# Optimization experiments

Measured on AMD Instinct MI355X. Metric: run time of the kernel, lower is better.

## Reference

```python
import jax, jax.numpy as jnp
import numpy as np

TEMPERATURE = 0.1
EPS = 1e-8  # torch F.cosine_similarity denom clamp


def setup_inputs() -> dict:
    key = jax.random.key(0)
    k1, k2, k3 = jax.random.split(key, 3)
    B, M, D, K = 8, 256, 768, 100
    N = B * M
    transformer_outputs = jax.random.normal(k1, (B, M, D), dtype=jnp.float32)
    cnn_targets = jax.random.normal(k2, (B, M, D), dtype=jnp.float32)
    # uniform sampling with replacement over [0, N) excluding self (multinomial on uniform mask)
    r = jax.random.randint(k3, (N, K), 0, N - 1)
    i = jnp.arange(N)[:, None]
    neg_indices = (r + (r >= i)).astype(jnp.int32)
    return {"transformer_outputs": transformer_outputs, "cnn_targets": cnn_targets, "neg_indices": neg_indices}


def reference(transformer_outputs, cnn_targets, neg_indices):
    B, M, D = transformer_outputs.shape
    N = B * M
    preds = transformer_outputs.reshape(N, D)
    targets = cnn_targets.reshape(N, D)
    pn = preds / jnp.clip(jnp.linalg.norm(preds, axis=-1, keepdims=True), EPS)
    tn = targets / jnp.clip(jnp.linalg.norm(targets, axis=-1, keepdims=True), EPS)
    # all pairwise cosine sims [N, N]; positive on the diagonal, negatives gathered by index
    sim = pn @ tn.T
    pos = jnp.diagonal(sim)                                   # [N]
    neg = sim[jnp.arange(N)[:, None], neg_indices]            # [N, K]
    logits = jnp.concatenate([pos[:, None], neg], axis=1) / TEMPERATURE
    # cross-entropy with label 0 for every row
    loss = -jnp.mean(jax.nn.log_softmax(logits, axis=-1)[:, 0])
    return loss
```

## Files before the change

kernel.cpp:

```cpp
#include <hip/hip_runtime.h>
#include <hip/hip_bf16.h>
#include <math.h>

#define NROWS 2048
#define DDIM  768
#define KNEG  100
#define NLOGITS 101
#define MT 7
#define KW 6

typedef __attribute__((ext_vector_type(4))) float floatx4;

static constexpr float TEMP_INV = 10.0f;
static constexpr float EPS_NORM = 1e-8f;

__device__ __forceinline__ unsigned pack_fp8x4(float a, float b, float c, float d) {
    int u = 0;
    u = __builtin_amdgcn_cvt_pk_fp8_f32(a, b, u, false);
    u = __builtin_amdgcn_cvt_pk_fp8_f32(c, d, u, true);
    return (unsigned)u;
}

__global__ __launch_bounds__(256) void cl_prep_kernel(
        const float* __restrict__ targets,
        unsigned char* __restrict__ tn8) {
    const int wave = threadIdx.x >> 6, lane = threadIdx.x & 63;
    const int row = blockIdx.x * 4 + wave;
    const float4* tv = (const float4*)(targets + (size_t)row * DDIM);
    const float4 a0 = tv[2 * lane], a1 = tv[2 * lane + 1], b0 = tv[128 + lane];

    float ss = 0.f;
    ss = fmaf(a0.x, a0.x, ss); ss = fmaf(a0.y, a0.y, ss);
    ss = fmaf(a0.z, a0.z, ss); ss = fmaf(a0.w, a0.w, ss);
    ss = fmaf(a1.x, a1.x, ss); ss = fmaf(a1.y, a1.y, ss);
    ss = fmaf(a1.z, a1.z, ss); ss = fmaf(a1.w, a1.w, ss);
    ss = fmaf(b0.x, b0.x, ss); ss = fmaf(b0.y, b0.y, ss);
    ss = fmaf(b0.z, b0.z, ss); ss = fmaf(b0.w, b0.w, ss);
    #pragma unroll
    for (int off = 32; off > 0; off >>= 1) ss += __shfl_xor(ss, off);
    const float it = 1.0f / fmaxf(sqrtf(ss), EPS_NORM);

    const unsigned u0 = pack_fp8x4(a0.x * it, a0.y * it, a0.z * it, a0.w * it);
    const unsigned u1 = pack_fp8x4(a1.x * it, a1.y * it, a1.z * it, a1.w * it);
    const unsigned u2 = pack_fp8x4(b0.x * it, b0.y * it, b0.z * it, b0.w * it);

    __shared__ __align__(16) unsigned char buf[4][DDIM];
    *(uint2*)(&buf[wave][8 * lane]) = make_uint2(u0, u1);
    *(unsigned*)(&buf[wave][512 + 4 * lane]) = u2;
    __syncthreads();
    if (lane < 48)
        ((uint4*)(tn8 + (size_t)row * DDIM))[lane] = *(const uint4*)(&buf[wave][16 * lane]);
}

__global__ __launch_bounds__(256, 4) void cl_rowloss_kernel(
        const float* __restrict__ preds,
        const unsigned char* __restrict__ tn8,
        const int* __restrict__ neg_idx,
        float* __restrict__ row_loss) {
    const int i = blockIdx.x;
    const int tid = threadIdx.x;
    const int wave = tid >> 6, lane = tid & 63;

    __shared__ __align__(16) unsigned char Ab[3][16 * DDIM];
    __shared__ __align__(16) unsigned char pn8[DDIM];
    __shared__ __align__(16) float parts[4][MT * 16];
    __shared__ int idx_lds[MT * 16];
    __shared__ float sP[4];

    if (tid < MT * 16)
        idx_lds[tid] = (tid == 0 || tid > KNEG) ? i : neg_idx[(size_t)i * KNEG + tid - 1];
    __syncthreads();

    auto stage = [&](int t, int buf, int nchunk) {
        #pragma unroll
        for (int it = 0; it < 3; ++it) {
            const int g = it * 256 + wave * 64 + lane;
            if (g < nchunk) {
                const int r = g / 48, c = g - r * 48;
                const unsigned char* src = tn8 + (size_t)idx_lds[t * 16 + r] * DDIM
                                           + ((c ^ (r & 7)) << 4);
                __builtin_amdgcn_global_load_lds(
                    (const __attribute__((address_space(1))) void*)src,
                    (__attribute__((address_space(3))) void*)&Ab[buf][(it * 256 + wave * 64) << 4],
                    16, 0, 0);
            }
        }
    };

    float4 pv4;
    if (tid < 192)
        pv4 = ((const float4*)(preds + (size_t)i * DDIM))[tid];

    stage(0, 0, 768);
    stage(1, 1, 768);

    if (tid < 192) {
        float ss = 0.f;
        ss = fmaf(pv4.x, pv4.x, ss); ss = fmaf(pv4.y, pv4.y, ss);
        ss = fmaf(pv4.z, pv4.z, ss); ss = fmaf(pv4.w, pv4.w, ss);
        #pragma unroll
        for (int off = 32; off > 0; off >>= 1) ss += __shfl_xor(ss, off);
        if (lane == 0) sP[wave] = ss;
    }
    asm volatile("s_waitcnt lgkmcnt(0)" ::: "memory");
    __builtin_amdgcn_s_barrier();
    __builtin_amdgcn_sched_barrier(0);

    if (tid < 192) {
        const float inv = 1.0f / fmaxf(sqrtf(sP[0] + sP[1] + sP[2]), EPS_NORM);
        ((unsigned*)pn8)[tid] = pack_fp8x4(pv4.x * inv, pv4.y * inv,
                                           pv4.z * inv, pv4.w * inv);
    }
    asm volatile("s_waitcnt lgkmcnt(0)" ::: "memory");
    __builtin_amdgcn_s_barrier();
    __builtin_amdgcn_sched_barrier(0);

    const int kb = wave * KW;
    const int q = lane >> 4;
    long long bfr[KW];
    #pragma unroll
    for (int kk = 0; kk < KW; ++kk)
        bfr[kk] = *(const long long*)(&pn8[(kb + kk) * 32 + q * 8]);

    const int aoff = (lane & 15) * DDIM + kb * 32 + q * 8;
    const int axor = (lane & 7) << 4;

    floatx4 acc[MT] = {};

#define CL_ITER(T, NWAIT, NC)                                                 \
    {                                                                         \
        if ((T) + 2 < MT) stage((T) + 2, ((T) + 2) % 3, NC);                  \
        asm volatile("s_waitcnt vmcnt(" #NWAIT ")" ::: "memory");             \
        __builtin_amdgcn_s_barrier();                                         \
        __builtin_amdgcn_sched_barrier(0);                                    \
        _Pragma("unroll")                                                     \
        for (int kk = 0; kk < KW; ++kk) {                                     \
            const long long af =                                              \
                *(const long long*)(&Ab[(T) % 3][(aoff + kk * 32) ^ axor]);   \
            acc[T] = __builtin_amdgcn_mfma_f32_16x16x32_fp8_fp8(af, bfr[kk],  \
                                                                acc[T], 0, 0, 0); \
        }                                                                     \
        asm volatile("s_waitcnt lgkmcnt(0)" ::: "memory");                    \
        __builtin_amdgcn_s_barrier();                                         \
        __builtin_amdgcn_sched_barrier(0);                                    \
    }

    CL_ITER(0, 6, 768)
    CL_ITER(1, 6, 768)
    CL_ITER(2, 6, 768)
    CL_ITER(3, 6, 768)
    CL_ITER(4, 4, 240)
    CL_ITER(5, 1, 0)
    CL_ITER(6, 0, 0)
#undef CL_ITER

    if ((lane & 15) == 0) {
        const int rb = q * 4;
        #pragma unroll
        for (int t = 0; t < MT; ++t)
            *(floatx4*)(&parts[wave][t * 16 + rb]) = acc[t];
    }
    __syncthreads();

    if (wave == 0) {
        const float v0 = (parts[0][lane] + parts[1][lane] +
                          parts[2][lane] + parts[3][lane]) * TEMP_INV;
        float v1 = -INFINITY;
        if (lane <= NLOGITS - 65)
            v1 = (parts[0][64 + lane] + parts[1][64 + lane] +
                  parts[2][64 + lane] + parts[3][64 + lane]) * TEMP_INV;
        const float l0 = __shfl(v0, 0);
        float m = fmaxf(v0, v1);
        #pragma unroll
        for (int off = 32; off > 0; off >>= 1) m = fmaxf(m, __shfl_xor(m, off));
        float e = expf(v0 - m);
        if (lane <= NLOGITS - 65) e += expf(v1 - m);
        #pragma unroll
        for (int off = 32; off > 0; off >>= 1) e += __shfl_xor(e, off);
        if (lane == 0) row_loss[i] = (m + logf(e)) - l0;
    }
}

__global__ void cl_reduce_kernel(const float* __restrict__ row_loss,
                                 float* __restrict__ out) {
    const int tid = threadIdx.x;
    float s = 0.f;
    #pragma unroll
    for (int c = 0; c < 2; ++c) {
        const float4 v = ((const float4*)row_loss)[tid + 256 * c];
        s += (v.x + v.y) + (v.z + v.w);
    }
    #pragma unroll
    for (int off = 32; off > 0; off >>= 1) s += __shfl_down(s, off);
    __shared__ float sw[4];
    const int wave = tid >> 6, lane = tid & 63;
    if (lane == 0) sw[wave] = s;
    __syncthreads();
    if (tid == 0) out[0] = (sw[0] + sw[1] + sw[2] + sw[3]) / (float)NROWS;
}

extern "C" void kernel_launch(void* const* d_in, const int* in_sizes, int n_in,
                              void* d_out, int out_size, void* d_ws, size_t ws_size,
                              hipStream_t stream) {
    const float* preds   = (const float*)d_in[0];
    const float* targets = (const float*)d_in[1];
    const int*   neg_idx = (const int*)d_in[2];
    float* out = (float*)d_out;

    unsigned char* tn8 = (unsigned char*)d_ws;
    float* row_loss = (float*)((char*)d_ws + (size_t)NROWS * DDIM);

    cl_prep_kernel<<<NROWS / 4, 256, 0, stream>>>(targets, tn8);
    cl_rowloss_kernel<<<NROWS, 256, 0, stream>>>(preds, tn8, neg_idx, row_loss);
    cl_reduce_kernel<<<1, 256, 0, stream>>>(row_loss, out);
}
```

Baseline: 25.67 us.

## Quantize normalized targets to FP4 and use scaled 16x16x128 MFMA

```diff
diff --git a/kernel.cpp b/kernel.cpp
--- a/kernel.cpp
+++ b/kernel.cpp
@@ -4,14 +4,16 @@
 
 #define NROWS 2048
 #define DDIM  768
+#define TNB   384
 #define KNEG  100
 #define NLOGITS 101
 #define MT 7
-#define KW 6
 
 typedef __attribute__((ext_vector_type(4))) float floatx4;
-
-static constexpr float TEMP_INV = 10.0f;
+typedef __attribute__((ext_vector_type(4))) int   intx4;
+typedef __attribute__((ext_vector_type(8))) int   intx8;
+
+static constexpr float LFAC = 10.0f / 32.0f;
 static constexpr float EPS_NORM = 1e-8f;
 
 __device__ __forceinline__ unsigned pack_fp8x4(float a, float b, float c, float d) {
@@ -21,9 +23,16 @@
     return (unsigned)u;
 }
 
+__device__ __forceinline__ unsigned fp4n(float v) {
+    const float a = fminf(fabsf(v), 6.0f);
+    const unsigned c = (a >= 0.25f) + (a >= 0.75f) + (a >= 1.25f) + (a >= 1.75f)
+                     + (a >= 2.5f)  + (a >= 3.5f)  + (a >= 5.0f);
+    return c | (v < 0.f ? 8u : 0u);
+}
+
 __global__ __launch_bounds__(256) void cl_prep_kernel(
         const float* __restrict__ targets,
-        unsigned char* __restrict__ tn8) {
+        unsigned char* __restrict__ tn4) {
     const int wave = threadIdx.x >> 6, lane = threadIdx.x & 63;
     const int row = blockIdx.x * 4 + wave;
     const float4* tv = (const float4*)(targets + (size_t)row * DDIM);
@@ -38,47 +47,54 @@
     ss = fmaf(b0.z, b0.z, ss); ss = fmaf(b0.w, b0.w, ss);
     #pragma unroll
     for (int off = 32; off > 0; off >>= 1) ss += __shfl_xor(ss, off);
-    const float it = 1.0f / fmaxf(sqrtf(ss), EPS_NORM);
-
-    const unsigned u0 = pack_fp8x4(a0.x * it, a0.y * it, a0.z * it, a0.w * it);
-    const unsigned u1 = pack_fp8x4(a1.x * it, a1.y * it, a1.z * it, a1.w * it);
-    const unsigned u2 = pack_fp8x4(b0.x * it, b0.y * it, b0.z * it, b0.w * it);
-
-    __shared__ __align__(16) unsigned char buf[4][DDIM];
-    *(uint2*)(&buf[wave][8 * lane]) = make_uint2(u0, u1);
-    *(unsigned*)(&buf[wave][512 + 4 * lane]) = u2;
-    __syncthreads();
-    if (lane < 48)
-        ((uint4*)(tn8 + (size_t)row * DDIM))[lane] = *(const uint4*)(&buf[wave][16 * lane]);
-}
-
-__global__ __launch_bounds__(256, 4) void cl_rowloss_kernel(
+    const float sc = 32.0f / fmaxf(sqrtf(ss), EPS_NORM);
+
+    const unsigned ua =  fp4n(a0.x * sc)        | (fp4n(a0.y * sc) << 4)
+                      | (fp4n(a0.z * sc) << 8)  | (fp4n(a0.w * sc) << 12)
+                      | (fp4n(a1.x * sc) << 16) | (fp4n(a1.y * sc) << 20)
+                      | (fp4n(a1.z * sc) << 24) | (fp4n(a1.w * sc) << 28);
+    const unsigned short ub = (unsigned short)(fp4n(b0.x * sc)
+                      | (fp4n(b0.y * sc) << 4) | (fp4n(b0.z * sc) << 8)
+                      | (fp4n(b0.w * sc) << 12));
+
+    __shared__ __align__(16) unsigned char buf[4][TNB];
+    *(unsigned*)(&buf[wave][4 * lane]) = ua;
+    *(unsigned short*)(&buf[wave][256 + 2 * lane]) = ub;
+    __syncthreads();
+    if (lane < 24)
+        ((uint4*)(tn4 + (size_t)row * TNB))[lane] = *(const uint4*)(&buf[wave][16 * lane]);
+}
+
+__global__ __launch_bounds__(256, 5) void cl_rowloss_kernel(
         const float* __restrict__ preds,
-        const unsigned char* __restrict__ tn8,
+        const unsigned char* __restrict__ tn4,
         const int* __restrict__ neg_idx,
         float* __restrict__ row_loss) {
     const int i = blockIdx.x;
     const int tid = threadIdx.x;
     const int wave = tid >> 6, lane = tid & 63;
-
-    __shared__ __align__(16) unsigned char Ab[3][16 * DDIM];
+    const int khalf = wave & 1, thalf = wave >> 1;
+    const int q = lane >> 4, rr = lane & 15;
+
+    __shared__ __align__(16) unsigned char Ab[2][32 * TNB];
     __shared__ __align__(16) unsigned char pn8[DDIM];
-    __shared__ __align__(16) float parts[4][MT * 16];
+    __shared__ __align__(16) float parts[2][MT * 16];
     __shared__ int idx_lds[MT * 16];
-    __shared__ float sP[4];
+    __shared__ float sP[3];
 
     if (tid < MT * 16)
         idx_lds[tid] = (tid == 0 || tid > KNEG) ? i : neg_idx[(size_t)i * KNEG + tid - 1];
     __syncthreads();
 
-    auto stage = [&](int t, int buf, int nchunk) {
+    auto stage = [&](int s, int buf, int nchunk) {
         #pragma unroll
         for (int it = 0; it < 3; ++it) {
             const int g = it * 256 + wave * 64 + lane;
             if (g < nchunk) {
-                const int r = g / 48, c = g - r * 48;
-                const unsigned char* src = tn8 + (size_t)idx_lds[t * 16 + r] * DDIM
-                                           + ((c ^ (r & 7)) << 4);
+                const int rl = g / 24, c = g - rl * 24;
+                const int slot = s * 16 + (rl < 16 ? rl : rl + 48);
+                const unsigned char* src = tn4 + (size_t)idx_lds[slot] * TNB
+                                           + ((c ^ (rl & 7)) << 4);
                 __builtin_amdgcn_global_load_lds(
                     (const __attribute__((address_space(1))) void*)src,
                     (__attribute__((address_space(3))) void*)&Ab[buf][(it * 256 + wave * 64) << 4],
@@ -88,16 +104,12 @@
     };
 
     float4 pv4;
-    if (tid < 192)
-        pv4 = ((const float4*)(preds + (size_t)i * DDIM))[tid];
-
+    if (tid < 192) pv4 = ((const float4*)(preds + (size_t)i * DDIM))[tid];
     stage(0, 0, 768);
-    stage(1, 1, 768);
 
     if (tid < 192) {
-        float ss = 0.f;
-        ss = fmaf(pv4.x, pv4.x, ss); ss = fmaf(pv4.y, pv4.y, ss);
-        ss = fmaf(pv4.z, pv4.z, ss); ss = fmaf(pv4.w, pv4.w, ss);
+        float ss = fmaf(pv4.x, pv4.x, fmaf(pv4.y, pv4.y,
+                   fmaf(pv4.z, pv4.z, pv4.w * pv4.w)));
         #pragma unroll
         for (int off = 32; off > 0; off >>= 1) ss += __shfl_xor(ss, off);
         if (lane == 0) sP[wave] = ss;
@@ -105,70 +117,68 @@
     asm volatile("s_waitcnt lgkmcnt(0)" ::: "memory");
     __builtin_amdgcn_s_barrier();
     __builtin_amdgcn_sched_barrier(0);
-
     if (tid < 192) {
         const float inv = 1.0f / fmaxf(sqrtf(sP[0] + sP[1] + sP[2]), EPS_NORM);
         ((unsigned*)pn8)[tid] = pack_fp8x4(pv4.x * inv, pv4.y * inv,
                                            pv4.z * inv, pv4.w * inv);
     }
-    asm volatile("s_waitcnt lgkmcnt(0)" ::: "memory");
-    __builtin_amdgcn_s_barrier();
-    __builtin_amdgcn_sched_barrier(0);
-
-    const int kb = wave * KW;
-    const int q = lane >> 4;
-    long long bfr[KW];
-    #pragma unroll
-    for (int kk = 0; kk < KW; ++kk)
-        bfr[kk] = *(const long long*)(&pn8[(kb + kk) * 32 + q * 8]);
-
-    const int aoff = (lane & 15) * DDIM + kb * 32 + q * 8;
-    const int axor = (lane & 7) << 4;
-
-    floatx4 acc[MT] = {};
-
-#define CL_ITER(T, NWAIT, NC)                                                 \
+    __syncthreads();
+
+    intx8 b8[3];
+    #pragma unroll
+    for (int m = 0; m < 3; ++m) {
+        const int boff = khalf * 384 + m * 128 + q * 32;
+        const intx4 lo = *(const intx4*)(&pn8[boff]);
+        const intx4 hi = *(const intx4*)(&pn8[boff + 16]);
+        b8[m] = (intx8){lo.x, lo.y, lo.z, lo.w, hi.x, hi.y, hi.z, hi.w};
+    }
+
+    floatx4 acc[4] = {};
+    const int rbase = (thalf * 16 + rr) * TNB;
+    const int rx = rr & 7;
+
+#define CL_S(S, NC_NEXT, DO_STAGE)                                            \
     {                                                                         \
-        if ((T) + 2 < MT) stage((T) + 2, ((T) + 2) % 3, NC);                  \
-        asm volatile("s_waitcnt vmcnt(" #NWAIT ")" ::: "memory");             \
-        __builtin_amdgcn_s_barrier();                                         \
-        __builtin_amdgcn_sched_barrier(0);                                    \
-        _Pragma("unroll")                                                     \
-        for (int kk = 0; kk < KW; ++kk) {                                     \
-            const long long af =                                              \
-                *(const long long*)(&Ab[(T) % 3][(aoff + kk * 32) ^ axor]);   \
-            acc[T] = __builtin_amdgcn_mfma_f32_16x16x32_fp8_fp8(af, bfr[kk],  \
-                                                                acc[T], 0, 0, 0); \
+        if (DO_STAGE) stage((S) + 1, ((S) + 1) & 1, NC_NEXT);                 \
+        if (!thalf || (S) < 3) {                                              \
+            _Pragma("unroll")                                                 \
+            for (int m = 0; m < 3; ++m) {                                     \
+                const int cl = khalf * 12 + m * 4 + q;                        \
+                const intx4 a4 = *(const intx4*)(&Ab[(S) & 1][rbase + ((cl ^ rx) << 4)]); \
+                const intx8 a8 = (intx8){a4.x, a4.y, a4.z, a4.w, 0, 0, 0, 0}; \
+                acc[S] = __builtin_amdgcn_mfma_scale_f32_16x16x128_f8f6f4(    \
+                    a8, b8[m], acc[S], 4 , 0 ,              \
+                    0, 127, 0, 127);                                          \
+            }                                                                 \
         }                                                                     \
-        asm volatile("s_waitcnt lgkmcnt(0)" ::: "memory");                    \
-        __builtin_amdgcn_s_barrier();                                         \
-        __builtin_amdgcn_sched_barrier(0);                                    \
-    }
-
-    CL_ITER(0, 6, 768)
-    CL_ITER(1, 6, 768)
-    CL_ITER(2, 6, 768)
-    CL_ITER(3, 6, 768)
-    CL_ITER(4, 4, 240)
-    CL_ITER(5, 1, 0)
-    CL_ITER(6, 0, 0)
-#undef CL_ITER
-
-    if ((lane & 15) == 0) {
+        __syncthreads();                                                      \
+    }
+
+    CL_S(0, 768, 1)
+    CL_S(1, 768, 1)
+    CL_S(2, 384, 1)
+    CL_S(3, 0, 0)
+#undef CL_S
+
+    if (rr == 0) {
         const int rb = q * 4;
-        #pragma unroll
-        for (int t = 0; t < MT; ++t)
-            *(floatx4*)(&parts[wave][t * 16 + rb]) = acc[t];
+        if (!thalf) {
+            #pragma unroll
+            for (int t = 0; t < 4; ++t)
+                *(floatx4*)(&parts[khalf][t * 16 + rb]) = acc[t];
+        } else {
+            #pragma unroll
+            for (int t = 0; t < 3; ++t)
+                *(floatx4*)(&parts[khalf][(t + 4) * 16 + rb]) = acc[t];
+        }
     }
     __syncthreads();
 
     if (wave == 0) {
-        const float v0 = (parts[0][lane] + parts[1][lane] +
-                          parts[2][lane] + parts[3][lane]) * TEMP_INV;
+        const float v0 = (parts[0][lane] + parts[1][lane]) * LFAC;
         float v1 = -INFINITY;
         if (lane <= NLOGITS - 65)
-            v1 = (parts[0][64 + lane] + parts[1][64 + lane] +
-                  parts[2][64 + lane] + parts[3][64 + lane]) * TEMP_INV;
+            v1 = (parts[0][64 + lane] + parts[1][64 + lane]) * LFAC;
         const float l0 = __shfl(v0, 0);
         float m = fmaxf(v0, v1);
         #pragma unroll
@@ -207,10 +217,10 @@
     const int*   neg_idx = (const int*)d_in[2];
     float* out = (float*)d_out;
 
-    unsigned char* tn8 = (unsigned char*)d_ws;
-    float* row_loss = (float*)((char*)d_ws + (size_t)NROWS * DDIM);
-
-    cl_prep_kernel<<<NROWS / 4, 256, 0, stream>>>(targets, tn8);
-    cl_rowloss_kernel<<<NROWS, 256, 0, stream>>>(preds, tn8, neg_idx, row_loss);
+    unsigned char* tn4 = (unsigned char*)d_ws;
+    float* row_loss = (float*)((char*)d_ws + (size_t)NROWS * TNB);
+
+    cl_prep_kernel<<<NROWS / 4, 256, 0, stream>>>(targets, tn4);
+    cl_rowloss_kernel<<<NROWS, 256, 0, stream>>>(preds, tn4, neg_idx, row_loss);
     cl_reduce_kernel<<<1, 256, 0, stream>>>(row_loss, out);
 }
```

Result: faster. 21.16 us (median of 2 runs) (-17.6%).
